# Kernel optimization log

Measured on AMD Instinct MI355X. Metric: run time of the kernel, lower is better.

The kernel has to match this reference:

```python
import jax, jax.numpy as jnp
import numpy as np

D_MODEL = 768
N_HEADS = 12
D_HEAD = 64
INIT_RANGE = 0.02
IGNORE = -100000.0


def setup_inputs() -> dict:
    key = jax.random.key(0)
    ks = jax.random.split(key, 5)
    x = jax.random.normal(ks[0], (2, 2048, D_MODEL), dtype=jnp.float32)
    W_Q = INIT_RANGE * jax.random.normal(ks[1], (N_HEADS, D_MODEL, D_HEAD), dtype=jnp.float32)
    W_K = INIT_RANGE * jax.random.normal(ks[2], (N_HEADS, D_MODEL, D_HEAD), dtype=jnp.float32)
    W_V = INIT_RANGE * jax.random.normal(ks[3], (N_HEADS, D_MODEL, D_HEAD), dtype=jnp.float32)
    W_O = INIT_RANGE * jax.random.normal(ks[4], (N_HEADS, D_HEAD, D_MODEL), dtype=jnp.float32)
    b_Q = jnp.zeros((N_HEADS, D_HEAD), dtype=jnp.float32)
    b_K = jnp.zeros((N_HEADS, D_HEAD), dtype=jnp.float32)
    b_V = jnp.zeros((N_HEADS, D_HEAD), dtype=jnp.float32)
    b_O = jnp.zeros((D_MODEL,), dtype=jnp.float32)
    return {"x": x, "W_Q": W_Q, "b_Q": b_Q, "W_K": W_K, "b_K": b_K,
            "W_V": W_V, "b_V": b_V, "W_O": W_O, "b_O": b_O}


def reference(x, W_Q, b_Q, W_K, b_K, W_V, b_V, W_O, b_O):
    # x: [b, s, m]; W_*: [h, m, d]
    Q = jnp.einsum('bsm,hmd->bshd', x, W_Q) + b_Q  # [b, s, h, d]
    K = jnp.einsum('bsm,hmd->bshd', x, W_K) + b_K
    V = jnp.einsum('bsm,hmd->bshd', x, W_V) + b_V
    scores = jnp.einsum('bqhd,bkhd->bhqk', Q, K) / jnp.sqrt(jnp.float32(D_HEAD))
    s = scores.shape[-1]
    causal = jnp.triu(jnp.ones((s, s), dtype=bool), k=1)  # True above diagonal
    scores = jnp.where(causal, jnp.float32(IGNORE), scores)
    pattern = jax.nn.softmax(scores, axis=-1)  # [b, h, q, k]
    Z = jnp.einsum('bhqk,bkhd->bqhd', pattern, V)
    out = jnp.einsum('bqhd,hdm->bqm', Z, W_O) + b_O
    return out
```

## Files before the change

### kernel.cpp

```cpp
#include <hip/hip_runtime.h>
#include <hip/hip_bf16.h>

#define BATCH 2
#define SLEN 2048
#define NH 12
#define DM 768
#define DH 64
#define ROWS (BATCH*SLEN)
#define NQKV (3*DM)
#define NCHUNK 40

typedef __attribute__((ext_vector_type(8))) short bf16x8;
typedef __attribute__((ext_vector_type(4))) float f32x4;
typedef __attribute__((ext_vector_type(16))) float f32x16;
typedef unsigned short u16;
typedef unsigned int u32;
typedef __attribute__((ext_vector_type(4))) unsigned short u16x4;
typedef __attribute__((ext_vector_type(8))) unsigned short u16x8;

__device__ __forceinline__ u16 f2b(float f) {
    unsigned int u = __builtin_bit_cast(unsigned int, f);
    unsigned int r = (u + 0x7FFFu + ((u >> 16) & 1u)) >> 16;
    return (u16)r;
}
__device__ __forceinline__ float b2f(u16 v) {
    unsigned int u = ((unsigned int)v) << 16;
    return __builtin_bit_cast(float, u);
}

__device__ __forceinline__ void gload16(const u16* g, u16* l) {
    __builtin_amdgcn_global_load_lds(
        (const __attribute__((address_space(1))) unsigned int*)g,
        (__attribute__((address_space(3))) unsigned int*)l,
        16, 0, 0);
}


__global__ __launch_bounds__(256) void pack_all(const float* __restrict__ x,
                                                const float* __restrict__ WQ, const float* __restrict__ WK,
                                                const float* __restrict__ WV, const float* __restrict__ WO,
                                                u16* __restrict__ xb, u16* __restrict__ wqkv,
                                                u16* __restrict__ wo) {
    __shared__ u16 L[64 * 72];
    int blk = blockIdx.x;
    int t = threadIdx.x;
    if (blk < 1536) {
        int i = blk * 256 + t;
        const float4* xv = (const float4*)x;
        float4 a = xv[i * 2], b = xv[i * 2 + 1];
        u16x8 o;
        o[0] = f2b(a.x); o[1] = f2b(a.y); o[2] = f2b(a.z); o[3] = f2b(a.w);
        o[4] = f2b(b.x); o[5] = f2b(b.y); o[6] = f2b(b.z); o[7] = f2b(b.w);
        *(u16x8*)(xb + (size_t)i * 8) = o;
    } else if (blk < 1968) {
        int idx = blk - 1536;
        int mt = idx % 12, h = (idx / 12) % 12, sel = idx / 144;
        const float* W = sel == 0 ? WQ : (sel == 1 ? WK : WV);
        const float* src = W + ((size_t)h * DM + mt * 64) * DH;
        for (int j = 0; j < 4; j++) {
            int i = t + 256 * j;
            int r = i >> 4, cf = i & 15;
            float4 v = ((const float4*)src)[i];
            u16x4 o; o[0] = f2b(v.x); o[1] = f2b(v.y); o[2] = f2b(v.z); o[3] = f2b(v.w);
            *(u16x4*)&L[r * 72 + cf * 4] = o;
        }
        __syncthreads();
        u16* orow = wqkv + ((size_t)(sel * DM + h * DH)) * DM + mt * 64;
        for (int j = 0; j < 16; j++) {
            int e = t + 256 * j;
            int d = e >> 6, mm = e & 63;
            orow[(size_t)d * DM + mm] = L[mm * 72 + d];
        }
    } else {
        int idx = blk - 1968;
        int bi = idx % 12, bj = idx / 12;
        for (int j = 0; j < 4; j++) {
            int i = t + 256 * j;
            int r = i >> 4, cf = i & 15;
            float4 v = ((const float4*)(WO + (size_t)(bi * 64 + r) * DM + bj * 64))[cf];
            u16x4 o; o[0] = f2b(v.x); o[1] = f2b(v.y); o[2] = f2b(v.z); o[3] = f2b(v.w);
            *(u16x4*)&L[r * 72 + cf * 4] = o;
        }
        __syncthreads();
        for (int j = 0; j < 16; j++) {
            int e = t + 256 * j;
            int c = e >> 6, r = e & 63;
            wo[(size_t)(bj * 64 + c) * DM + bi * 64 + r] = L[r * 72 + c];
        }
    }
}


__global__ __launch_bounds__(256) void gemm_qkv(const u16* __restrict__ A, const u16* __restrict__ Bt,
                                                const float* __restrict__ bQ, const float* __restrict__ bK,
                                                const float* __restrict__ bV,
                                                u16* __restrict__ Qb, u16* __restrict__ Kb, u16* __restrict__ Vb) {
    __shared__ u16 Al[128 * 64];
    __shared__ u16 Bl[96 * 64];
    int t = threadIdx.x;
    int n0 = blockIdx.x * 96, m0 = blockIdx.y * 128;
    int lane = t & 63, w = t >> 6;
    int ln = lane & 15, qd = lane >> 4;
    int wr = (w & 1) * 64, wc = (w >> 1) * 48;
    int srow = lane >> 3, slot = lane & 7;
    f32x4 acc[4][3] = {};

    for (int kt = 0; kt < DM / 64; kt++) {
        __syncthreads();
        for (int j = 0; j < 4; j++) {
            int r = w * 32 + j * 8 + srow;
            int gc = slot ^ (r & 7);
            gload16(A + (size_t)(m0 + r) * DM + kt * 64 + gc * 8, &Al[(w * 32 + j * 8) * 64]);
        }
        for (int j = 0; j < 3; j++) {
            int r = w * 24 + j * 8 + srow;
            int gc = slot ^ (r & 7);
            gload16(Bt + (size_t)(n0 + r) * DM + kt * 64 + gc * 8, &Bl[(w * 24 + j * 8) * 64]);
        }
        __syncthreads();
        for (int ks = 0; ks < 2; ks++) {
            int sl = ((ks * 4 + qd) ^ (ln & 7)) * 8;
            bf16x8 af[4], bfr[3];
            for (int rt = 0; rt < 4; rt++)
                af[rt] = *(const bf16x8*)&Al[(wr + rt * 16 + ln) * 64 + sl];
            for (int ct = 0; ct < 3; ct++)
                bfr[ct] = *(const bf16x8*)&Bl[(wc + ct * 16 + ln) * 64 + sl];
            for (int rt = 0; rt < 4; rt++)
                for (int ct = 0; ct < 3; ct++)
                    acc[rt][ct] = __builtin_amdgcn_mfma_f32_16x16x32_bf16(af[rt], bfr[ct], acc[rt][ct], 0, 0, 0);
        }
    }
    int sel = n0 / DM;
    if (sel == 2) {
        for (int ct = 0; ct < 3; ct++) {
            int col = n0 - 2 * DM + wc + ct * 16 + ln;
            int hh = col >> 6, dd = col & 63;
            float bv = bV[col];
            for (int rt = 0; rt < 4; rt++) {
                int row = m0 + wr + rt * 16 + qd * 4;
                int bb = row >> 11, ss = row & 2047;
                u16x4 pk;
                for (int r = 0; r < 4; r++) pk[r] = f2b(acc[rt][ct][r] + bv);
                *(u16x4*)&Vb[(((size_t)bb * NH + hh) * DH + dd) * SLEN + ss] = pk;
            }
        }
    } else {
        const float* bias = sel == 0 ? bQ : bK;
        u16* Out = sel == 0 ? Qb : Kb;
        const float qs = sel == 0 ? 0.125f * 1.44269504f : 1.0f;
        for (int ct = 0; ct < 3; ct++) {
            int col = n0 - sel * DM + wc + ct * 16 + ln;
            int hh = col >> 6, dd = col & 63;
            float bv = bias[col];
            for (int rt = 0; rt < 4; rt++) {
                int row = m0 + wr + rt * 16 + qd * 4;
                for (int r = 0; r < 4; r++) {
                    int rg = row + r;
                    int bb = rg >> 11, ss = rg & 2047;
                    Out[(((size_t)bb * NH + hh) * SLEN + ss) * DH + dd] = f2b((acc[rt][ct][r] + bv) * qs);
                }
            }
        }
    }
}


__device__ __forceinline__ void cid2qc(int cid, int& qt, int& c, int& nc) {
    if (cid < 4)       { qt = cid;                   c = 0;               nc = 1; }
    else if (cid < 12) { qt = 4 + ((cid - 4) >> 1);  c = (cid - 4) & 1;   nc = 2; }
    else if (cid < 24) { qt = 8 + (cid - 12) / 3;    c = (cid - 12) % 3;  nc = 3; }
    else               { qt = 12 + ((cid - 24) >> 2); c = (cid - 24) & 3; nc = 4; }
}

__global__ __launch_bounds__(256, 4) void attn(const u16* __restrict__ Qb, const u16* __restrict__ Kb,
                                               const u16* __restrict__ Vtg,
                                               u16* __restrict__ Po, float* __restrict__ Plv) {
    __shared__ u16 Kl[64 * 64];
    __shared__ u16 Vt[64 * 64];
    __shared__ u16 Pq[4][32 * 72];
    int blk = blockIdx.x;
    int cid = (NCHUNK - 1) - blk / 24;
    int j24 = blk % 24;
    int bh = (j24 & 7) * 3 + (j24 >> 3);
    int qt, c, nc;
    cid2qc(cid, qt, c, nc);
    int ntiles = 2 * qt + 2;
    int kt0 = c * ntiles / nc, kt1 = (c + 1) * ntiles / nc;
    const u16* Qp = Qb + (size_t)bh * SLEN * DH;
    const u16* Kp = Kb + (size_t)bh * SLEN * DH;
    const u16* Vp = Vtg + (size_t)bh * SLEN * DH;
    int t = threadIdx.x, lane = t & 63, w = t >> 6;
    int l31 = lane & 31, h = lane >> 5;
    int qg = qt * 128 + w * 32 + l31;
    int srow = lane >> 3, slot = lane & 7;

    bf16x8 qf[4];
    for (int ks = 0; ks < 4; ks++)
        qf[ks] = *(const bf16x8*)(Qp + (size_t)qg * DH + ks * 16 + h * 8);

    bf16x8 onesf;
    for (int e = 0; e < 8; e++) onesf[e] = (short)0x3F80;

    f32x16 o[2] = {};
    f32x16 oL = {};
    u16* Pw = Pq[w];

    for (int kt = kt0; kt < kt1; kt++) {
        int k0 = kt * 64;
        __syncthreads();
        for (int j = 0; j < 2; j++) {
            int r = w * 16 + j * 8 + srow;
            int gc = slot ^ (r & 7);
            gload16(Kp + (size_t)(k0 + r) * DH + gc * 8, &Kl[(w * 16 + j * 8) * 64]);
            gload16(Vp + (size_t)r * SLEN + k0 + gc * 8, &Vt[(w * 16 + j * 8) * 64]);
        }
        __syncthreads();

        for (int kb = 0; kb < 2; kb++) {
            f32x16 sf = {};
            for (int ks = 0; ks < 4; ks++) {
                int row = kb * 32 + l31;
                bf16x8 kf = *(const bf16x8*)&Kl[row * 64 + (((ks * 2 + h) ^ (row & 7)) * 8)];
                sf = __builtin_amdgcn_mfma_f32_32x32x16_bf16(kf, qf[ks], sf, 0, 0, 0);
            }
            if (k0 + 63 > qt * 128 + w * 32) {
                for (int r = 0; r < 16; r++) {
                    int kg = k0 + kb * 32 + (r & 3) + 8 * (r >> 2) + 4 * h;
                    if (kg > qg) sf[r] = -1e30f;
                }
            }
            u32 pr[8];
            for (int p = 0; p < 8; p++) {
                u32 e0 = __builtin_bit_cast(u32, exp2f(sf[2 * p]));
                u32 e1 = __builtin_bit_cast(u32, exp2f(sf[2 * p + 1]));
                pr[p] = __builtin_amdgcn_perm(e1, e0, 0x07060302u);
            }
            {
                uint2 s;
                s.x = pr[0]; s.y = pr[1];
                *(uint2*)&Pw[l31 * 72 + kb * 32 + 4 * h] = s;
                s.x = pr[2]; s.y = pr[3];
                *(uint2*)&Pw[l31 * 72 + kb * 32 + 8 + 4 * h] = s;
                s.x = pr[4]; s.y = pr[5];
                *(uint2*)&Pw[l31 * 72 + kb * 32 + 16 + 4 * h] = s;
                s.x = pr[6]; s.y = pr[7];
                *(uint2*)&Pw[l31 * 72 + kb * 32 + 24 + 4 * h] = s;
            }
            for (int cc = 0; cc < 2; cc++) {
                bf16x8 pf = *(const bf16x8*)&Pw[l31 * 72 + kb * 32 + cc * 16 + 8 * h];
                int ch4 = kb * 2 + cc;
                oL = __builtin_amdgcn_mfma_f32_32x32x16_bf16(onesf, pf, oL, 0, 0, 0);
                for (int db = 0; db < 2; db++) {
                    int row = db * 32 + l31;
                    bf16x8 vf = *(const bf16x8*)&Vt[row * 64 + (((ch4 * 2 + h) ^ (row & 7)) * 8)];
                    o[db] = __builtin_amdgcn_mfma_f32_32x32x16_bf16(vf, pf, o[db], 0, 0, 0);
                }
            }
        }
    }

    size_t pid = (size_t)bh * NCHUNK + cid;
    u16* op = Po + pid * (128 * 64);
    for (int db = 0; db < 2; db++)
        for (int rq = 0; rq < 4; rq++) {
            u16x4 ov;
            for (int j = 0; j < 4; j++) ov[j] = f2b(o[db][rq * 4 + j]);
            *(u16x4*)&op[(w * 32 + l31) * 64 + db * 32 + rq * 8 + 4 * h] = ov;
        }
    if (h == 0)
        Plv[pid * 128 + w * 32 + l31] = oL[0];
}


__global__ __launch_bounds__(256) void combine(const u16* __restrict__ Po, const float* __restrict__ Plv,
                                               u16* __restrict__ Zb) {
    int qtile = blockIdx.x, bh = blockIdx.y;
    int b = bh / NH, hH = bh % NH;
    int nc = qtile < 4 ? 1 : (qtile < 8 ? 2 : (qtile < 12 ? 3 : 4));
    int base = qtile < 4 ? qtile
             : (qtile < 8 ? 4 + (qtile - 4) * 2
             : (qtile < 12 ? 12 + (qtile - 8) * 3
                           : 24 + (qtile - 12) * 4));
    int t = threadIdx.x;
    int q = t >> 1, dseg = (t & 1) * 32;

    float acc[32] = {};
    float lsum = 0.f;
    for (int cc = 0; cc < nc; cc++) {
        size_t pid = (size_t)bh * NCHUNK + base + cc;
        lsum += Plv[pid * 128 + q];
        const u16* op = Po + pid * (128 * 64) + q * 64 + dseg;
        for (int jj = 0; jj < 4; jj++) {
            u16x8 v = *(const u16x8*)(op + jj * 8);
            for (int e = 0; e < 8; e++)
                acc[jj * 8 + e] += b2f(v[e]);
        }
    }
    float inv = 1.0f / lsum;
    u16* Zp = Zb + ((size_t)b * SLEN + qtile * 128 + q) * DM + hH * DH + dseg;
    for (int jj = 0; jj < 4; jj++) {
        u16x8 ov;
        for (int e = 0; e < 8; e++) ov[e] = f2b(acc[jj * 8 + e] * inv);
        *(u16x8*)(Zp + jj * 8) = ov;
    }
}


__global__ __launch_bounds__(256) void gemm_proj(const u16* __restrict__ A, const u16* __restrict__ Bt,
                                                 const float* __restrict__ bO, float* __restrict__ out) {
    __shared__ u16 Al[64 * 64];
    __shared__ u16 Bl[96 * 64];
    int t = threadIdx.x;
    int n0 = blockIdx.x * 96, m0 = blockIdx.y * 64;
    int lane = t & 63, w = t >> 6;
    int ln = lane & 15, qd = lane >> 4;
    int wr = (w & 1) * 32, wc = (w >> 1) * 48;
    int srow = lane >> 3, slot = lane & 7;
    f32x4 acc[2][3] = {};

    for (int kt = 0; kt < DM / 64; kt++) {
        __syncthreads();
        for (int j = 0; j < 2; j++) {
            int r = w * 16 + j * 8 + srow;
            int gc = slot ^ (r & 7);
            gload16(A + (size_t)(m0 + r) * DM + kt * 64 + gc * 8, &Al[(w * 16 + j * 8) * 64]);
        }
        for (int j = 0; j < 3; j++) {
            int r = w * 24 + j * 8 + srow;
            int gc = slot ^ (r & 7);
            gload16(Bt + (size_t)(n0 + r) * DM + kt * 64 + gc * 8, &Bl[(w * 24 + j * 8) * 64]);
        }
        __syncthreads();
        for (int ks = 0; ks < 2; ks++) {
            int sl = ((ks * 4 + qd) ^ (ln & 7)) * 8;
            bf16x8 af[2], bfr[3];
            for (int rt = 0; rt < 2; rt++)
                af[rt] = *(const bf16x8*)&Al[(wr + rt * 16 + ln) * 64 + sl];
            for (int ct = 0; ct < 3; ct++)
                bfr[ct] = *(const bf16x8*)&Bl[(wc + ct * 16 + ln) * 64 + sl];
            for (int rt = 0; rt < 2; rt++)
                for (int ct = 0; ct < 3; ct++)
                    acc[rt][ct] = __builtin_amdgcn_mfma_f32_16x16x32_bf16(af[rt], bfr[ct], acc[rt][ct], 0, 0, 0);
        }
    }
    for (int ct = 0; ct < 3; ct++) {
        int col = n0 + wc + ct * 16 + ln;
        float bv = bO[col];
        for (int rt = 0; rt < 2; rt++) {
            int row = m0 + wr + rt * 16 + qd * 4;
            for (int r = 0; r < 4; r++)
                out[(size_t)(row + r) * DM + col] = acc[rt][ct][r] + bv;
        }
    }
}


extern "C" void kernel_launch(void* const* d_in, const int* in_sizes, int n_in,
                              void* d_out, int out_size, void* d_ws, size_t ws_size,
                              hipStream_t stream) {
    const float* x  = (const float*)d_in[0];
    const float* WQ = (const float*)d_in[1];
    const float* bQ = (const float*)d_in[2];
    const float* WK = (const float*)d_in[3];
    const float* bK = (const float*)d_in[4];
    const float* WV = (const float*)d_in[5];
    const float* bV = (const float*)d_in[6];
    const float* WO = (const float*)d_in[7];
    const float* bO = (const float*)d_in[8];
    float* out = (float*)d_out;

    u16* xb   = (u16*)d_ws;
    u16* wqkv = xb + (size_t)ROWS * DM;
    u16* wo   = wqkv + (size_t)NQKV * DM;
    u16* Qb   = wo + (size_t)DM * DM;
    size_t hsz = (size_t)BATCH * NH * SLEN * DH;
    u16* Kb   = Qb + hsz;
    u16* Vb   = Kb + hsz;
    u16* Zb   = Vb + hsz;
    u16* Po   = Zb + (size_t)ROWS * DM;
    float* Pl = (float*)(Po + (size_t)BATCH * NH * NCHUNK * 128 * 64);

    pack_all<<<2112, 256, 0, stream>>>(x, WQ, WK, WV, WO, xb, wqkv, wo);
    gemm_qkv<<<dim3(NQKV / 96, ROWS / 128), 256, 0, stream>>>(xb, wqkv, bQ, bK, bV, Qb, Kb, Vb);
    attn<<<dim3(NCHUNK * 24), 256, 0, stream>>>(Qb, Kb, Vb, Po, Pl);
    combine<<<dim3(SLEN / 128, BATCH * NH), 256, 0, stream>>>(Po, Pl, Zb);
    gemm_proj<<<dim3(DM / 96, ROWS / 64), 256, 0, stream>>>(Zb, wo, bO, out);
}
```

Measured before the change: 160.1 us.

## Double-buffer K/V tiles in attention and stage V-projection stores through shared memory

The attention kernel now double-buffers the K and V tiles in shared memory, prefetching the next tile while computing the current one, and needs only one barrier per iteration. It replaces the MFMA row-sum with a scalar accumulation of the bf16 probabilities plus a cross-half shuffle, and swaps the padded P buffer for an XOR-swizzled layout. The QKV GEMM epilogue for V writes through shared memory so the transposed global stores are 16-byte and contiguous. The larger shared-memory footprint lowers the occupancy hint from 4 to 3 blocks, and the scalar row-sum adds VALU work.

Measured after the change: 165.2 us. 3.1% more time.

```diff
diff --git a/kernel.cpp b/kernel.cpp
--- a/kernel.cpp
+++ b/kernel.cpp
@@ -95,8 +95,9 @@
                                                 const float* __restrict__ bQ, const float* __restrict__ bK,
                                                 const float* __restrict__ bV,
                                                 u16* __restrict__ Qb, u16* __restrict__ Kb, u16* __restrict__ Vb) {
-    __shared__ u16 Al[128 * 64];
-    __shared__ u16 Bl[96 * 64];
+    __shared__ u16 S[128 * 64 + 96 * 64];
+    u16* Al = S;
+    u16* Bl = S + 128 * 64;
     int t = threadIdx.x;
     int n0 = blockIdx.x * 96, m0 = blockIdx.y * 128;
     int lane = t & 63, w = t >> 6;
@@ -132,17 +133,25 @@
     }
     int sel = n0 / DM;
     if (sel == 2) {
+        __syncthreads();
         for (int ct = 0; ct < 3; ct++) {
-            int col = n0 - 2 * DM + wc + ct * 16 + ln;
-            int hh = col >> 6, dd = col & 63;
-            float bv = bV[col];
+            int c = wc + ct * 16 + ln;
+            float bv = bV[n0 - 2 * DM + c];
             for (int rt = 0; rt < 4; rt++) {
-                int row = m0 + wr + rt * 16 + qd * 4;
-                int bb = row >> 11, ss = row & 2047;
-                u16x4 pk;
-                for (int r = 0; r < 4; r++) pk[r] = f2b(acc[rt][ct][r] + bv);
-                *(u16x4*)&Vb[(((size_t)bb * NH + hh) * DH + dd) * SLEN + ss] = pk;
-            }
+                int s = wr + rt * 16 + qd * 4;
+                for (int r = 0; r < 4; r++)
+                    S[c * 136 + s + r] = f2b(acc[rt][ct][r] + bv);
+            }
+        }
+        __syncthreads();
+        int bb = m0 >> 11, ss0 = m0 & 2047;
+        for (int it = 0; it < 6; it++) {
+            int e = t + it * 256;
+            int c = e >> 4, ck = e & 15;
+            int gcol = n0 - 2 * DM + c;
+            int hh = gcol >> 6, dd = gcol & 63;
+            u16x8 v = *(const u16x8*)&S[c * 136 + ck * 8];
+            *(u16x8*)&Vb[(((size_t)bb * NH + hh) * DH + dd) * SLEN + ss0 + ck * 8] = v;
         }
     } else {
         const float* bias = sel == 0 ? bQ : bK;
@@ -172,12 +181,12 @@
     else               { qt = 12 + ((cid - 24) >> 2); c = (cid - 24) & 3; nc = 4; }
 }
 
-__global__ __launch_bounds__(256, 4) void attn(const u16* __restrict__ Qb, const u16* __restrict__ Kb,
+__global__ __launch_bounds__(256, 3) void attn(const u16* __restrict__ Qb, const u16* __restrict__ Kb,
                                                const u16* __restrict__ Vtg,
                                                u16* __restrict__ Po, float* __restrict__ Plv) {
-    __shared__ u16 Kl[64 * 64];
-    __shared__ u16 Vt[64 * 64];
-    __shared__ u16 Pq[4][32 * 72];
+    __shared__ u16 Kl[2][64 * 64];
+    __shared__ u16 Vt[2][64 * 64];
+    __shared__ u16 Pq[4][32 * 64];
     int blk = blockIdx.x;
     int cid = (NCHUNK - 1) - blk / 24;
     int j24 = blk % 24;
@@ -193,34 +202,40 @@
     int l31 = lane & 31, h = lane >> 5;
     int qg = qt * 128 + w * 32 + l31;
     int srow = lane >> 3, slot = lane & 7;
+    int sw = (l31 & 7) << 3;
 
     bf16x8 qf[4];
     for (int ks = 0; ks < 4; ks++)
         qf[ks] = *(const bf16x8*)(Qp + (size_t)qg * DH + ks * 16 + h * 8);
 
-    bf16x8 onesf;
-    for (int e = 0; e < 8; e++) onesf[e] = (short)0x3F80;
-
     f32x16 o[2] = {};
-    f32x16 oL = {};
+    float lsum = 0.f;
     u16* Pw = Pq[w];
 
-    for (int kt = kt0; kt < kt1; kt++) {
+    auto stage = [&](int kt, int buf) {
         int k0 = kt * 64;
-        __syncthreads();
         for (int j = 0; j < 2; j++) {
             int r = w * 16 + j * 8 + srow;
             int gc = slot ^ (r & 7);
-            gload16(Kp + (size_t)(k0 + r) * DH + gc * 8, &Kl[(w * 16 + j * 8) * 64]);
-            gload16(Vp + (size_t)r * SLEN + k0 + gc * 8, &Vt[(w * 16 + j * 8) * 64]);
-        }
-        __syncthreads();
+            gload16(Kp + (size_t)(k0 + r) * DH + gc * 8, &Kl[buf][(w * 16 + j * 8) * 64]);
+            gload16(Vp + (size_t)r * SLEN + k0 + gc * 8, &Vt[buf][(w * 16 + j * 8) * 64]);
+        }
+    };
+
+    stage(kt0, 0);
+    __syncthreads();
+    int cur = 0;
+    for (int kt = kt0; kt < kt1; kt++) {
+        int k0 = kt * 64;
+        if (kt + 1 < kt1) stage(kt + 1, cur ^ 1);
+        const u16* Kc = Kl[cur];
+        const u16* Vc = Vt[cur];
 
         for (int kb = 0; kb < 2; kb++) {
             f32x16 sf = {};
             for (int ks = 0; ks < 4; ks++) {
                 int row = kb * 32 + l31;
-                bf16x8 kf = *(const bf16x8*)&Kl[row * 64 + (((ks * 2 + h) ^ (row & 7)) * 8)];
+                bf16x8 kf = *(const bf16x8*)&Kc[row * 64 + (((ks * 2 + h) ^ (row & 7)) * 8)];
                 sf = __builtin_amdgcn_mfma_f32_32x32x16_bf16(kf, qf[ks], sf, 0, 0, 0);
             }
             if (k0 + 63 > qt * 128 + w * 32) {
@@ -235,28 +250,33 @@
                 u32 e1 = __builtin_bit_cast(u32, exp2f(sf[2 * p + 1]));
                 pr[p] = __builtin_amdgcn_perm(e1, e0, 0x07060302u);
             }
+            for (int p = 0; p < 8; p++) {
+                lsum += __builtin_bit_cast(float, pr[p] << 16);
+                lsum += __builtin_bit_cast(float, pr[p] & 0xFFFF0000u);
+            }
             {
                 uint2 s;
                 s.x = pr[0]; s.y = pr[1];
-                *(uint2*)&Pw[l31 * 72 + kb * 32 + 4 * h] = s;
+                *(uint2*)&Pw[l31 * 64 + ((kb * 32 + 4 * h) ^ sw)] = s;
                 s.x = pr[2]; s.y = pr[3];
-                *(uint2*)&Pw[l31 * 72 + kb * 32 + 8 + 4 * h] = s;
+                *(uint2*)&Pw[l31 * 64 + ((kb * 32 + 8 + 4 * h) ^ sw)] = s;
                 s.x = pr[4]; s.y = pr[5];
-                *(uint2*)&Pw[l31 * 72 + kb * 32 + 16 + 4 * h] = s;
+                *(uint2*)&Pw[l31 * 64 + ((kb * 32 + 16 + 4 * h) ^ sw)] = s;
                 s.x = pr[6]; s.y = pr[7];
-                *(uint2*)&Pw[l31 * 72 + kb * 32 + 24 + 4 * h] = s;
+                *(uint2*)&Pw[l31 * 64 + ((kb * 32 + 24 + 4 * h) ^ sw)] = s;
             }
             for (int cc = 0; cc < 2; cc++) {
-                bf16x8 pf = *(const bf16x8*)&Pw[l31 * 72 + kb * 32 + cc * 16 + 8 * h];
+                bf16x8 pf = *(const bf16x8*)&Pw[l31 * 64 + ((kb * 32 + cc * 16 + 8 * h) ^ sw)];
                 int ch4 = kb * 2 + cc;
-                oL = __builtin_amdgcn_mfma_f32_32x32x16_bf16(onesf, pf, oL, 0, 0, 0);
                 for (int db = 0; db < 2; db++) {
                     int row = db * 32 + l31;
-                    bf16x8 vf = *(const bf16x8*)&Vt[row * 64 + (((ch4 * 2 + h) ^ (row & 7)) * 8)];
+                    bf16x8 vf = *(const bf16x8*)&Vc[row * 64 + (((ch4 * 2 + h) ^ (row & 7)) * 8)];
                     o[db] = __builtin_amdgcn_mfma_f32_32x32x16_bf16(vf, pf, o[db], 0, 0, 0);
                 }
             }
         }
+        __syncthreads();
+        cur ^= 1;
     }
 
     size_t pid = (size_t)bh * NCHUNK + cid;
@@ -267,8 +287,9 @@
             for (int j = 0; j < 4; j++) ov[j] = f2b(o[db][rq * 4 + j]);
             *(u16x4*)&op[(w * 32 + l31) * 64 + db * 32 + rq * 8 + 4 * h] = ov;
         }
+    lsum += __shfl_xor(lsum, 32, 64);
     if (h == 0)
-        Plv[pid * 128 + w * 32 + l31] = oL[0];
+        Plv[pid * 128 + w * 32 + l31] = lsum;
 }
 
 
```
